# Kernel tuning notes

Hardware: AMD Instinct MI355X
Metric: run time of the kernel (lower is better)

The kernel has to match this reference:

```python
import jax, jax.numpy as jnp
import numpy as np

# Module constants derived from init_kwargs (order=3, N_fft=1536, N_hop=384,
# low_f0=62.5, high_f0=500, stride=3, fs=48000, mode='linear', center=False)
PAD = 768          # int(fs//low_f0)*(order-1)//2
FRAME = 3072       # frame_size
HOP = 384          # N_hop
NFFT = 1536
K = 1537           # conv kernel length = 2*max_delay+1
NPITCH = 226       # N_freqs + 1


def _comb_filter_weights():
    """Replicates comb_filter.init_weights for the default config."""
    fs, max_delay, stride = 48000, 768, 3
    delays = np.linspace(stride, max_delay, max_delay // stride)[::-1]
    freqs = fs / delays
    lo = np.abs(freqs - 62.5).argmin()
    hi = np.abs(freqs - 500.0).argmin()
    filter_delays = delays[lo:hi + 1].astype('int')  # 225 delays
    order = 3
    fw = np.hanning(order + 2)
    fw = (fw / fw.sum())[1:-1].astype('float32')  # 3 taps
    weights = np.zeros([NPITCH, K], dtype=np.float32)
    mid = K // 2
    for i in range(len(filter_delays)):
        d = int(filter_delays[i])
        weights[i, mid] = fw[order // 2]
        if mid + d - 1 <= K - 1:
            weights[i, mid + d - 1] = fw[order // 2 + 1]
        if mid - d + 1 >= 0:
            weights[i, mid - d + 1] = fw[order // 2 - 1]
    weights[-1, mid] = 1.0  # identity (unvoiced) filter
    weights = weights / weights.sum(axis=-1, keepdims=True)
    return jnp.asarray(weights)


def setup_inputs() -> dict:
    key = jax.random.key(0)
    k1, k2 = jax.random.split(key)
    x = jax.random.normal(k1, (2, 192000), dtype=jnp.float32)
    pitch = jax.random.randint(k2, (2, 497), 0, NPITCH, dtype=jnp.int32)
    conv_w = _comb_filter_weights()  # (226, 1537) - the learned Conv2d weight
    return {"x": x, "pitch": pitch, "conv_w": conv_w}


def reference(x, pitch, conv_w):
    bs = x.shape[0]
    xp = jnp.pad(x, ((0, 0), (PAD, PAD)))  # ConstantPad1d
    T = (xp.shape[1] - FRAME) // HOP + 1   # number of frames (497)
    idx = jnp.arange(T)[:, None] * HOP + jnp.arange(FRAME)[None, :]
    frames = xp[:, idx]                    # (bs, T, FRAME) == Unfold
    # dense multi-filter 1D conv over each frame: (bs*T, 226, 1536)
    inp = frames.reshape(bs * T, 1, FRAME)
    kern = conv_w[:, None, :]              # (226, 1, 1537) OIH
    filt = jax.lax.conv_general_dilated(
        inp, kern, window_strides=(1,), padding='VALID',
        dimension_numbers=('NCH', 'OIH', 'NCH'))
    # hann window (torch.hann_window, periodic)
    window = 0.5 - 0.5 * jnp.cos(2.0 * jnp.pi * jnp.arange(NFFT, dtype=filt.dtype) / NFFT)
    filt = filt * window[None, None, :]
    filt = filt.reshape(bs, T, NPITCH, NFFT)
    # one-hot pitch selection (the MoE-style routing step)
    oh = jax.nn.one_hot(pitch, NPITCH, dtype=filt.dtype)  # (bs, T, 226)
    out = jnp.einsum('btfl,btf->btl', filt, oh)           # (bs, T, 1536)
    return out[..., None]                                  # (bs, T, 1536, 1)
```

## Files before the change

kernel.cpp:

```cpp
#include <hip/hip_runtime.h>
#include <hip/hip_bf16.h>


#define BATCH   2
#define XLEN    192000
#define PADW    768
#define FRAME   3072
#define HOP     384
#define NFFT    1536
#define KW      1537
#define TFRAMES 497
#define MAXTAP  8

__global__ __launch_bounds__(256) void comb_filter_kernel(
        const float* __restrict__ x,
        const int* __restrict__ pitch,
        const float* __restrict__ conv_w,
        float* __restrict__ out) {
    const int bt = blockIdx.x;
    const int b  = bt / TFRAMES;
    const int t  = bt - b * TFRAMES;

    __shared__ int   s_ntap;
    __shared__ int   s_tap_k[MAXTAP];
    __shared__ float s_tap_w[MAXTAP];
    if (threadIdx.x == 0) s_ntap = 0;
    __syncthreads();

    const int p = pitch[bt];
    const float* wrow = conv_w + (long)p * KW;
    for (int k = threadIdx.x; k < KW; k += blockDim.x) {
        float w = wrow[k];
        if (w != 0.0f) {
            int slot = atomicAdd(&s_ntap, 1);
            if (slot < MAXTAP) { s_tap_k[slot] = k; s_tap_w[slot] = w; }
        }
    }
    __syncthreads();

    const int nt = min(s_ntap, MAXTAP);
    const long xbase = (long)b * XLEN;
    const int  off0  = t * HOP - PADW;
    const float inv_nfft = 1.0f / (float)NFFT;
    float* orow = out + (long)bt * NFFT;

    for (int l = threadIdx.x; l < NFFT; l += blockDim.x) {
        float acc = 0.0f;
        #pragma unroll 4
        for (int j = 0; j < nt; ++j) {
            int xi = off0 + l + s_tap_k[j];
            float xv = (xi >= 0 && xi < XLEN) ? x[xbase + xi] : 0.0f;
            acc = fmaf(s_tap_w[j], xv, acc);
        }
        float win = 0.5f - 0.5f * cosf(6.283185307179586f * (float)l * inv_nfft);
        orow[l] = acc * win;
    }
}

extern "C" void kernel_launch(void* const* d_in, const int* in_sizes, int n_in,
                              void* d_out, int out_size, void* d_ws, size_t ws_size,
                              hipStream_t stream) {
    const float* x      = (const float*)d_in[0];
    const int*   pitch  = (const int*)d_in[1];
    const float* conv_w = (const float*)d_in[2];
    float*       out    = (float*)d_out;

    dim3 grid(BATCH * TFRAMES);
    dim3 block(256);
    comb_filter_kernel<<<grid, block, 0, stream>>>(x, pitch, conv_w, out);
}
```

Measured before the change: 69.94 us.

## Stage frame window in shared memory and vectorize output with float4

```diff
diff --git a/kernel.cpp b/kernel.cpp
--- a/kernel.cpp
+++ b/kernel.cpp
@@ -11,6 +11,7 @@
 #define KW      1537
 #define TFRAMES 497
 #define MAXTAP  8
+#define SWIN    3072
 
 __global__ __launch_bounds__(256) void comb_filter_kernel(
         const float* __restrict__ x,
@@ -20,16 +21,35 @@
     const int bt = blockIdx.x;
     const int b  = bt / TFRAMES;
     const int t  = bt - b * TFRAMES;
+    const int tid = threadIdx.x;
 
+    __shared__ float s_x[SWIN];
     __shared__ int   s_ntap;
     __shared__ int   s_tap_k[MAXTAP];
     __shared__ float s_tap_w[MAXTAP];
-    if (threadIdx.x == 0) s_ntap = 0;
+    if (tid == 0) s_ntap = 0;
     __syncthreads();
+
+    const long xbase = (long)b * XLEN;
+    const int  off0  = t * HOP - PADW;
+
+    for (int v = tid; v < SWIN / 4; v += 256) {
+        const int base = off0 + v * 4;
+        float4 val;
+        if (base >= 0 && base + 3 < XLEN) {
+            val = *(const float4*)(x + xbase + base);
+        } else {
+            val.x = (base + 0 >= 0 && base + 0 < XLEN) ? x[xbase + base + 0] : 0.0f;
+            val.y = (base + 1 >= 0 && base + 1 < XLEN) ? x[xbase + base + 1] : 0.0f;
+            val.z = (base + 2 >= 0 && base + 2 < XLEN) ? x[xbase + base + 2] : 0.0f;
+            val.w = (base + 3 >= 0 && base + 3 < XLEN) ? x[xbase + base + 3] : 0.0f;
+        }
+        *(float4*)(s_x + v * 4) = val;
+    }
 
     const int p = pitch[bt];
     const float* wrow = conv_w + (long)p * KW;
-    for (int k = threadIdx.x; k < KW; k += blockDim.x) {
+    for (int k = tid; k < KW; k += 256) {
         float w = wrow[k];
         if (w != 0.0f) {
             int slot = atomicAdd(&s_ntap, 1);
@@ -39,21 +59,26 @@
     __syncthreads();
 
     const int nt = min(s_ntap, MAXTAP);
-    const long xbase = (long)b * XLEN;
-    const int  off0  = t * HOP - PADW;
-    const float inv_nfft = 1.0f / (float)NFFT;
+    const float w2pi = 6.283185307179586f / (float)NFFT;
     float* orow = out + (long)bt * NFFT;
 
-    for (int l = threadIdx.x; l < NFFT; l += blockDim.x) {
-        float acc = 0.0f;
-        #pragma unroll 4
+    for (int v = tid; v < NFFT / 4; v += 256) {
+        const int l = v * 4;
+        float4 acc = make_float4(0.f, 0.f, 0.f, 0.f);
+        #pragma unroll 3
         for (int j = 0; j < nt; ++j) {
-            int xi = off0 + l + s_tap_k[j];
-            float xv = (xi >= 0 && xi < XLEN) ? x[xbase + xi] : 0.0f;
-            acc = fmaf(s_tap_w[j], xv, acc);
+            const int   kk = s_tap_k[j];
+            const float w  = s_tap_w[j];
+            acc.x = fmaf(w, s_x[l + 0 + kk], acc.x);
+            acc.y = fmaf(w, s_x[l + 1 + kk], acc.y);
+            acc.z = fmaf(w, s_x[l + 2 + kk], acc.z);
+            acc.w = fmaf(w, s_x[l + 3 + kk], acc.w);
         }
-        float win = 0.5f - 0.5f * cosf(6.283185307179586f * (float)l * inv_nfft);
-        orow[l] = acc * win;
+        acc.x *= 0.5f - 0.5f * __cosf(w2pi * (float)(l + 0));
+        acc.y *= 0.5f - 0.5f * __cosf(w2pi * (float)(l + 1));
+        acc.z *= 0.5f - 0.5f * __cosf(w2pi * (float)(l + 2));
+        acc.w *= 0.5f - 0.5f * __cosf(w2pi * (float)(l + 3));
+        *(float4*)(orow + l) = acc;
     }
 }
 
```

After: 65.59 us. -6.2%, faster.
